# Optimization experiments

Hardware: AMD Instinct MI355X
Metric: run time of the kernel (lower is better)

Reference implementation:

```python
import jax, jax.numpy as jnp
import numpy as np
import math

B, S, DIM, H, KVH = 2, 2048, 2048, 16, 4
HD = DIM // H          # 128
G = H // KVH           # 4 (GQA repeat factor)
NEG = -1e9             # fp32 additive mask value (matches torch path)


def _rotate_half(x):
    x1, x2 = jnp.split(x, 2, axis=-1)
    return jnp.concatenate([-x2, x1], axis=-1)


def setup_inputs() -> dict:
    key = jax.random.key(0)
    ks = jax.random.split(key, 8)
    hidden_states = jax.random.normal(ks[0], (B, S, DIM), jnp.float32)
    # standard RoPE tables [S, HD]
    inv_freq = 1.0 / (10000.0 ** (jnp.arange(0, HD, 2, dtype=jnp.float32) / HD))
    freqs = jnp.outer(jnp.arange(S, dtype=jnp.float32), inv_freq)
    emb = jnp.concatenate([freqs, freqs], axis=-1)
    position_cos = jnp.cos(emb)
    position_sin = jnp.sin(emb)
    alibi_bias = jax.random.normal(ks[1], (B, S, S), jnp.float32) * 0.01
    attention_mask = jnp.zeros((B, 1, 1, S), jnp.float32)
    sc = 0.02
    wq = jax.random.normal(ks[2], (DIM, DIM), jnp.float32) * sc
    wk = jax.random.normal(ks[3], (DIM, KVH * HD), jnp.float32) * sc
    wv = jax.random.normal(ks[4], (DIM, KVH * HD), jnp.float32) * sc
    wo = jax.random.normal(ks[5], (DIM, DIM), jnp.float32) * sc
    return {"hidden_states": hidden_states, "position_cos": position_cos,
            "position_sin": position_sin, "alibi_bias": alibi_bias,
            "attention_mask": attention_mask, "wq": wq, "wk": wk, "wv": wv, "wo": wo}


def reference(hidden_states, position_cos, position_sin, alibi_bias,
              attention_mask, wq, wk, wv, wo):
    b, s, d = hidden_states.shape
    # projections (weights stored as [in, out])
    q = (hidden_states @ wq).reshape(b, s, H, HD).transpose(0, 2, 1, 3)      # [B,H,S,HD]
    k = (hidden_states @ wk).reshape(b, s, KVH, HD).transpose(0, 2, 1, 3)    # [B,KVH,S,HD]
    v = (hidden_states @ wv).reshape(b, s, KVH, HD).transpose(0, 2, 1, 3)
    # RoPE
    cos = position_cos[None, None]  # [1,1,S,HD]
    sin = position_sin[None, None]
    q = q * cos + _rotate_half(q) * sin
    k = k * cos + _rotate_half(k) * sin
    # GQA repeat kv heads
    k = jnp.repeat(k, G, axis=1)   # [B,H,S,HD]
    v = jnp.repeat(v, G, axis=1)
    scores = jnp.einsum('bhqd,bhkd->bhqk', q, k) * (1.0 / math.sqrt(HD))
    causal = jnp.triu(jnp.full((s, s), NEG, jnp.float32), 1)
    scores = scores + causal + alibi_bias[:, None, :, :] + attention_mask
    attn = jax.nn.softmax(scores.astype(jnp.float32), axis=-1).astype(q.dtype)
    out = jnp.einsum('bhqk,bhkd->bhqd', attn, v)                              # [B,H,S,HD]
    out = out.transpose(0, 2, 1, 3).reshape(b, s, d)
    return out @ wo
```

## Files before the change

### kernel.cpp

```cpp
#include <hip/hip_runtime.h>
#include <hip/hip_bf16.h>

#define Bb   2
#define Ss   2048
#define Dd   2048
#define Hh   16
#define KVHh 4
#define HDd  128

typedef __bf16 bf16x8 __attribute__((ext_vector_type(8)));
typedef float f32x4 __attribute__((ext_vector_type(4)));

__device__ __forceinline__ unsigned short f2bf(float f) {
    unsigned u = __float_as_uint(f);
    unsigned r = (u + 0x7FFFu + ((u >> 16) & 1u)) >> 16;
    return (unsigned short)r;
}
__device__ __forceinline__ float bfu2f(unsigned short u) {
    return __uint_as_float(((unsigned)u) << 16);
}

#define GLOAD16(g, l) __builtin_amdgcn_global_load_lds( \
    (const __attribute__((address_space(1))) unsigned int*)(g), \
    (__attribute__((address_space(3))) unsigned int*)(l), 16, 0, 0)

__global__ __launch_bounds__(256)
void cast_bf16(const float* __restrict__ X, unsigned short* __restrict__ Y)
{
    int idx = blockIdx.x * 256 + threadIdx.x;
    float4 v = reinterpret_cast<const float4*>(X)[idx];
    ushort4 o;
    o.x = f2bf(v.x); o.y = f2bf(v.y); o.z = f2bf(v.z); o.w = f2bf(v.w);
    reinterpret_cast<ushort4*>(Y)[idx] = o;
}

__global__ __launch_bounds__(256)
void wt_cast(const float* __restrict__ W, unsigned short* __restrict__ WT,
             int K, int N)
{
    __shared__ float tile[32][33];
    int k0 = blockIdx.x * 32, n0 = blockIdx.y * 32;
    int tx = threadIdx.x & 31, ty = threadIdx.x >> 5;
    #pragma unroll
    for (int i = 0; i < 32; i += 8)
        tile[ty + i][tx] = W[(size_t)(k0 + ty + i) * N + n0 + tx];
    __syncthreads();
    #pragma unroll
    for (int i = 0; i < 32; i += 8)
        WT[(size_t)(n0 + ty + i) * K + k0 + tx] = f2bf(tile[tx][ty + i]);
}

template<bool BF16OUT>
__global__ __launch_bounds__(256)
void gemm_bt(const unsigned short* __restrict__ A,
             const unsigned short* __restrict__ BT,
             void* __restrict__ Cv, int M, int N, int K)
{
    __shared__ __align__(16) unsigned short sA[128 * 32];
    __shared__ __align__(16) unsigned short sB[128 * 32];
    const int tid  = threadIdx.x;
    const int wave = tid >> 6;
    const int lane = tid & 63;
    const int m    = lane & 15;
    const int quad = lane >> 4;
    const int wm   = wave >> 1, wn = wave & 1;
    const int m0   = blockIdx.y * 128, n0 = blockIdx.x * 128;

    const int srow = tid >> 2;
    const int skg  = (tid & 3) * 8;

    f32x4 acc[4][4];
    #pragma unroll
    for (int r = 0; r < 4; ++r)
        #pragma unroll
        for (int c = 0; c < 4; ++c) acc[r][c] = (f32x4){0.f, 0.f, 0.f, 0.f};

    const unsigned short* pa = A  + (size_t)(m0 + srow) * K + skg;
    const unsigned short* pb = BT + (size_t)(n0 + srow) * K + skg;
    unsigned short* la = &sA[wave * 16 * 32];
    unsigned short* lb = &sB[wave * 16 * 32];

    for (int k0 = 0; k0 < K; k0 += 32) {
        GLOAD16(pa + k0, la);
        GLOAD16(pa + (size_t)64 * K + k0, la + 64 * 32);
        GLOAD16(pb + k0, lb);
        GLOAD16(pb + (size_t)64 * K + k0, lb + 64 * 32);
        __syncthreads();
        bf16x8 af[4], bfr[4];
        #pragma unroll
        for (int r = 0; r < 4; ++r)
            af[r] = *reinterpret_cast<const bf16x8*>(
                &sA[(wm * 64 + r * 16 + m) * 32 + quad * 8]);
        #pragma unroll
        for (int c = 0; c < 4; ++c)
            bfr[c] = *reinterpret_cast<const bf16x8*>(
                &sB[(wn * 64 + c * 16 + m) * 32 + quad * 8]);
        #pragma unroll
        for (int r = 0; r < 4; ++r)
            #pragma unroll
            for (int c = 0; c < 4; ++c)
                acc[r][c] = __builtin_amdgcn_mfma_f32_16x16x32_bf16(
                    af[r], bfr[c], acc[r][c], 0, 0, 0);
        __syncthreads();
    }
    #pragma unroll
    for (int r = 0; r < 4; ++r)
        #pragma unroll
        for (int c = 0; c < 4; ++c)
            #pragma unroll
            for (int e = 0; e < 4; ++e) {
                size_t row = m0 + wm * 64 + r * 16 + quad * 4 + e;
                size_t col = n0 + wn * 64 + c * 16 + m;
                if (BF16OUT)
                    ((unsigned short*)Cv)[row * N + col] = f2bf(acc[r][c][e]);
                else
                    ((float*)Cv)[row * N + col] = acc[r][c][e];
            }
}

__global__ __launch_bounds__(256)
void rope_bf(unsigned short* __restrict__ X, const float* __restrict__ cosT,
             const float* __restrict__ sinT, int nhshift, int rowstride,
             float scale, int total)
{
    int idx = blockIdx.x * 256 + threadIdx.x;
    if (idx >= total) return;
    int i   = idx & 63;
    int rh  = idx >> 6;
    int row = rh >> nhshift;
    int h   = rh & ((1 << nhshift) - 1);
    int s   = row & (Ss - 1);
    unsigned short* xp = X + (size_t)row * rowstride + h * HDd;
    float x1 = bfu2f(xp[i]);
    float x2 = bfu2f(xp[i + 64]);
    float c1 = cosT[s * HDd + i];
    float c2 = cosT[s * HDd + i + 64];
    float s1 = sinT[s * HDd + i];
    float s2 = sinT[s * HDd + i + 64];
    xp[i]      = f2bf((x1 * c1 - x2 * s1) * scale);
    xp[i + 64] = f2bf((x2 * c2 + x1 * s2) * scale);
}

__global__ __launch_bounds__(256)
void vt_cast_bf(const unsigned short* __restrict__ KV,
                unsigned short* __restrict__ VT)
{
    __shared__ unsigned short tile[32][34];
    int st = blockIdx.x * 32, dt = blockIdx.y * 32;
    int bk = blockIdx.z;
    int b = bk >> 2, kvh = bk & 3;
    int tx = threadIdx.x & 31, ty = threadIdx.x >> 5;
    #pragma unroll
    for (int i = 0; i < 32; i += 8)
        tile[ty + i][tx] = KV[(size_t)(b * Ss + st + ty + i) * 1024 + 512 + kvh * HDd + dt + tx];
    __syncthreads();
    #pragma unroll
    for (int i = 0; i < 32; i += 8)
        VT[(((size_t)b * KVHh + kvh) * HDd + dt + ty + i) * Ss + st + tx] =
            tile[tx][ty + i];
}

__global__ __launch_bounds__(256, 2)
void flash_attn(const unsigned short* __restrict__ Qb,
                const unsigned short* __restrict__ KVb,
                const unsigned short* __restrict__ VT,
                const float* __restrict__ alibi,
                const float* __restrict__ amask,
                unsigned short* __restrict__ ctx)
{
    __shared__ __align__(16) unsigned short kbuf[3][32 * 128];
    __shared__ __align__(16) unsigned short vbuf[3][128 * 32];
    __shared__ __align__(16) float          abuf[3][16 * 32];
    __shared__ __align__(16) float          am_lds[Ss];
    __shared__ unsigned short s_p[4][16][56];

    const int tid  = threadIdx.x;
    const int w    = tid >> 6;
    const int lane = tid & 63;
    const int m    = lane & 15;
    const int quad = lane >> 4;

    const int kvh = blockIdx.y;
    const int b   = blockIdx.z;
    const int h   = kvh * 4 + w;

    const unsigned short* vt0 = VT + ((size_t)b * KVHh + kvh) * HDd * Ss;
    const float* amrow = amask + (size_t)b * Ss;

    const int krow_s = tid >> 4;
    const int koff_b = ((tid & 15) * 16) ^ ((krow_s & 7) << 4);
    const int vrow_s = tid >> 2;
    const int vchk_s = (tid & 3) ^ ((vrow_s >> 1) & 3);
    const int dstw   = w * 512;

    const unsigned short* kgbase = KVb + (size_t)b * Ss * 1024 + kvh * HDd;

    {
        const float* ag = amrow + tid * 4;
        GLOAD16(ag,        am_lds + w * 256);
        GLOAD16(ag + 1024, am_lds + 1024 + w * 256);
    }

    const int qts[2] = { (int)blockIdx.x, 127 - (int)blockIdx.x };

    #pragma unroll 1
    for (int pi = 0; pi < 2; ++pi) {
        const int q0 = qts[pi] * 16;

        bf16x8 qa[4];
        {
            const unsigned short* qrow = Qb + (size_t)(b * Ss + q0 + m) * Dd + h * HDd;
            #pragma unroll
            for (int c = 0; c < 4; ++c)
                qa[c] = *reinterpret_cast<const bf16x8*>(qrow + c * 32 + quad * 8);
        }

        f32x4 o[8];
        #pragma unroll
        for (int f = 0; f < 8; ++f) o[f] = (f32x4){0.f, 0.f, 0.f, 0.f};
        float lrow[4] = {0.f, 0.f, 0.f, 0.f};

        const float* arowB = alibi + ((size_t)b * Ss + q0) * Ss;
        const int ntiles = (q0 + 47) >> 5;

        auto STAGE = [&](int kn, int buf) {
            const unsigned short* kg =
                kgbase + (size_t)(kn + krow_s) * 1024 + (koff_b >> 1);
            GLOAD16(kg,             &kbuf[buf][dstw]);
            GLOAD16(kg + 16 * 1024, &kbuf[buf][2048 + dstw]);
            const unsigned short* vg = vt0 + (size_t)vrow_s * Ss + kn + vchk_s * 8;
            GLOAD16(vg,             &vbuf[buf][dstw]);
            GLOAD16(vg + 64 * Ss,   &vbuf[buf][2048 + dstw]);
            if (tid < 128) {
                const float* ag = arowB + (size_t)(tid >> 3) * Ss + kn + (tid & 7) * 4;
                GLOAD16(ag, &abuf[buf][w * 256]);
            }
        };

        STAGE(0, 0);
        asm volatile("s_waitcnt vmcnt(0)" ::: "memory");
        __syncthreads();

        int cur = 0;
        #pragma unroll 1
        for (int kt = 0; kt < ntiles; ++kt) {
            const int k0  = kt * 32;
            const int nxt = (cur == 2) ? 0 : cur + 1;

            if (kt + 1 < ntiles) {
                STAGE(k0 + 32, nxt);
                if (w < 2) asm volatile("s_waitcnt vmcnt(5)" ::: "memory");
                else       asm volatile("s_waitcnt vmcnt(4)" ::: "memory");
            } else {
                asm volatile("s_waitcnt vmcnt(0)" ::: "memory");
            }
            __builtin_amdgcn_s_barrier();
            __builtin_amdgcn_sched_barrier(0);

            const float am0 = am_lds[k0 + m];
            const float am1 = am_lds[k0 + 16 + m];

            const char* kb  = (const char*)&kbuf[cur][0];
            const char* vbp = (const char*)&vbuf[cur][0];
            const int  ksw  = (m & 7) << 4;
            const int  vsw  = ((m >> 1) & 3) << 4;
            bf16x8 kb0[4], kb1[4];
            #pragma unroll
            for (int c = 0; c < 4; ++c) {
                kb0[c] = *(const bf16x8*)(kb + m * 256        + ((c * 64 + quad * 16) ^ ksw));
                kb1[c] = *(const bf16x8*)(kb + (16 + m) * 256 + ((c * 64 + quad * 16) ^ ksw));
            }
            f32x4 s0 = {0.f, 0.f, 0.f, 0.f}, s1 = {0.f, 0.f, 0.f, 0.f};
            #pragma unroll
            for (int c = 0; c < 4; ++c) {
                s0 = __builtin_amdgcn_mfma_f32_16x16x32_bf16(qa[c], kb0[c], s0, 0, 0, 0);
                s1 = __builtin_amdgcn_mfma_f32_16x16x32_bf16(qa[c], kb1[c], s1, 0, 0, 0);
            }

            #pragma unroll
            for (int r = 0; r < 4; ++r) {
                const int row = quad * 4 + r;
                const int qi  = q0 + row;
                float x0 = s0[r] + abuf[cur][row * 32 + m]      + am0;
                float x1 = s1[r] + abuf[cur][row * 32 + 16 + m] + am1;
                x0 = (k0 + m      <= qi) ? x0 : -1e30f;
                x1 = (k0 + 16 + m <= qi) ? x1 : -1e30f;
                const float p0 = __expf(x0);
                const float p1 = __expf(x1);
                lrow[r] += p0 + p1;
                s_p[w][row][m]      = f2bf(p0);
                s_p[w][row][16 + m] = f2bf(p1);
            }
            __builtin_amdgcn_wave_barrier();
            const bf16x8 pa = *reinterpret_cast<const bf16x8*>(&s_p[w][m][quad * 8]);
            __builtin_amdgcn_wave_barrier();

            #pragma unroll
            for (int f = 0; f < 8; ++f) {
                const bf16x8 vb = *(const bf16x8*)(vbp + (f * 16 + m) * 64 +
                                                   ((quad * 16) ^ vsw));
                o[f] = __builtin_amdgcn_mfma_f32_16x16x32_bf16(pa, vb, o[f], 0, 0, 0);
            }

            cur = nxt;
        }

        float inv[4];
        #pragma unroll
        for (int r = 0; r < 4; ++r) {
            float l = lrow[r];
            l += __shfl_xor(l, 1, 64);
            l += __shfl_xor(l, 2, 64);
            l += __shfl_xor(l, 4, 64);
            l += __shfl_xor(l, 8, 64);
            inv[r] = 1.f / l;
        }
        #pragma unroll
        for (int f = 0; f < 8; ++f)
            #pragma unroll
            for (int r = 0; r < 4; ++r)
                ctx[(size_t)(b * Ss + q0 + quad * 4 + r) * Dd + h * HDd + f * 16 + m] =
                    f2bf(o[f][r] * inv[r]);

        __syncthreads();
    }
}

extern "C" void kernel_launch(void* const* d_in, const int* in_sizes, int n_in,
                              void* d_out, int out_size, void* d_ws, size_t ws_size,
                              hipStream_t stream) {
    const float* hidden = (const float*)d_in[0];
    const float* cosT   = (const float*)d_in[1];
    const float* sinT   = (const float*)d_in[2];
    const float* alibi  = (const float*)d_in[3];
    const float* amask  = (const float*)d_in[4];
    const float* wq     = (const float*)d_in[5];
    const float* wk     = (const float*)d_in[6];
    const float* wv     = (const float*)d_in[7];
    const float* wo     = (const float*)d_in[8];
    float* out = (float*)d_out;

    char* ws = (char*)d_ws;
    unsigned short* Abf   = (unsigned short*)(ws);
    unsigned short* wqT   = (unsigned short*)(ws + 16777216);
    unsigned short* kvT   = (unsigned short*)(ws + 25165824);
    unsigned short* woT   = (unsigned short*)(ws + 29360128);
    unsigned short* Qraw  = (unsigned short*)(ws + 37748736);
    unsigned short* KVraw = (unsigned short*)(ws + 54525952);
    unsigned short* VT    = (unsigned short*)(ws + 62914560);
    unsigned short* Ctx   = (unsigned short*)(ws + 67108864);

    const int M = Bb * Ss;

    cast_bf16<<<(M * Dd / 4) / 256, 256, 0, stream>>>(hidden, Abf);
    wt_cast<<<dim3(64, 64), 256, 0, stream>>>(wq, wqT, Dd, Dd);
    wt_cast<<<dim3(64, 16), 256, 0, stream>>>(wk, kvT, Dd, 512);
    wt_cast<<<dim3(64, 16), 256, 0, stream>>>(wv, kvT + (size_t)512 * Dd, Dd, 512);
    wt_cast<<<dim3(64, 64), 256, 0, stream>>>(wo, woT, Dd, Dd);

    gemm_bt<true><<<dim3(Dd / 128, M / 128), 256, 0, stream>>>(Abf, wqT, Qraw, M, Dd, Dd);
    gemm_bt<true><<<dim3(1024 / 128, M / 128), 256, 0, stream>>>(Abf, kvT, KVraw, M, 1024, Dd);

    const float scale = 0.08838834764831845f;
    int totQ = Bb * Ss * Hh * 64;
    rope_bf<<<totQ / 256, 256, 0, stream>>>(Qraw, cosT, sinT, 4, Dd, scale, totQ);
    int totK = Bb * Ss * KVHh * 64;
    rope_bf<<<totK / 256, 256, 0, stream>>>(KVraw, cosT, sinT, 2, 1024, 1.0f, totK);

    vt_cast_bf<<<dim3(Ss / 32, HDd / 32, Bb * KVHh), 256, 0, stream>>>(KVraw, VT);

    flash_attn<<<dim3(64, KVHh, Bb), 256, 0, stream>>>(Qraw, KVraw, VT, alibi, amask, Ctx);

    gemm_bt<false><<<dim3(Dd / 128, M / 128), 256, 0, stream>>>(Ctx, woT, out, M, Dd, Dd);
}
```

Baseline: 417.4 us.

## Fuse QKV projection, merge weight casts and RoPE, interleave paired query tiles

Merges the four weight-transpose launches into one kernel and the Q and KV projections into a single GEMM with a combined 3072-wide output. The two RoPE launches become one kernel over that shared buffer. The attention kernel now processes its two query tiles (short and long) together in one K/V loop, reusing each staged K/V tile and its fragments for both, and reorders block-to-tile mapping by batch. This cuts kernel launches and halves K/V LDS traffic for the short tile, at the cost of higher register pressure from two accumulator sets.

```diff
diff --git a/kernel.cpp b/kernel.cpp
--- a/kernel.cpp
+++ b/kernel.cpp
@@ -7,6 +7,7 @@
 #define Hh   16
 #define KVHh 4
 #define HDd  128
+#define QKVW 3072
 
 typedef __bf16 bf16x8 __attribute__((ext_vector_type(8)));
 typedef float f32x4 __attribute__((ext_vector_type(4)));
@@ -35,11 +36,19 @@
 }
 
 __global__ __launch_bounds__(256)
-void wt_cast(const float* __restrict__ W, unsigned short* __restrict__ WT,
-             int K, int N)
+void wt_cast_all(const float* __restrict__ wq, const float* __restrict__ wk,
+                 const float* __restrict__ wv, const float* __restrict__ wo,
+                 unsigned short* __restrict__ wqkvT, unsigned short* __restrict__ woT)
 {
     __shared__ float tile[32][33];
-    int k0 = blockIdx.x * 32, n0 = blockIdx.y * 32;
+    int id = blockIdx.x;
+    const float* W; unsigned short* WT; int N, kx, ny;
+    if (id < 4096)      {            W = wq; WT = wqkvT;                        N = 2048; kx = id & 63; ny = id >> 6; }
+    else if (id < 5120) { id -= 4096; W = wk; WT = wqkvT + (size_t)2048 * 2048; N = 512;  kx = id & 63; ny = id >> 6; }
+    else if (id < 6144) { id -= 5120; W = wv; WT = wqkvT + (size_t)2560 * 2048; N = 512;  kx = id & 63; ny = id >> 6; }
+    else                { id -= 6144; W = wo; WT = woT;                         N = 2048; kx = id & 63; ny = id >> 6; }
+    const int K = 2048;
+    int k0 = kx * 32, n0 = ny * 32;
     int tx = threadIdx.x & 31, ty = threadIdx.x >> 5;
     #pragma unroll
     for (int i = 0; i < 32; i += 8)
@@ -119,18 +128,15 @@
 }
 
 __global__ __launch_bounds__(256)
-void rope_bf(unsigned short* __restrict__ X, const float* __restrict__ cosT,
-             const float* __restrict__ sinT, int nhshift, int rowstride,
-             float scale, int total)
-{
-    int idx = blockIdx.x * 256 + threadIdx.x;
-    if (idx >= total) return;
-    int i   = idx & 63;
-    int rh  = idx >> 6;
-    int row = rh >> nhshift;
-    int h   = rh & ((1 << nhshift) - 1);
-    int s   = row & (Ss - 1);
-    unsigned short* xp = X + (size_t)row * rowstride + h * HDd;
+void rope_all(unsigned short* __restrict__ qkv, const float* __restrict__ cosT,
+              const float* __restrict__ sinT)
+{
+    const int h   = blockIdx.y;
+    const int row = blockIdx.x * 4 + (threadIdx.x >> 6);
+    const int i   = threadIdx.x & 63;
+    const int s   = row & (Ss - 1);
+    const float scale = (h < Hh) ? 0.08838834764831845f : 1.0f;
+    unsigned short* xp = qkv + (size_t)row * QKVW + h * HDd;
     float x1 = bfu2f(xp[i]);
     float x2 = bfu2f(xp[i + 64]);
     float c1 = cosT[s * HDd + i];
@@ -152,7 +158,7 @@
     int tx = threadIdx.x & 31, ty = threadIdx.x >> 5;
     #pragma unroll
     for (int i = 0; i < 32; i += 8)
-        tile[ty + i][tx] = KV[(size_t)(b * Ss + st + ty + i) * 1024 + 512 + kvh * HDd + dt + tx];
+        tile[ty + i][tx] = KV[(size_t)(b * Ss + st + ty + i) * QKVW + 2560 + kvh * HDd + dt + tx];
     __syncthreads();
     #pragma unroll
     for (int i = 0; i < 32; i += 8)
@@ -161,8 +167,7 @@
 }
 
 __global__ __launch_bounds__(256, 2)
-void flash_attn(const unsigned short* __restrict__ Qb,
-                const unsigned short* __restrict__ KVb,
+void flash_attn(const unsigned short* __restrict__ qkv,
                 const unsigned short* __restrict__ VT,
                 const float* __restrict__ alibi,
                 const float* __restrict__ amask,
@@ -170,22 +175,32 @@
 {
     __shared__ __align__(16) unsigned short kbuf[3][32 * 128];
     __shared__ __align__(16) unsigned short vbuf[3][128 * 32];
-    __shared__ __align__(16) float          abuf[3][16 * 32];
+    __shared__ __align__(16) float          abuf[3][2][512];
     __shared__ __align__(16) float          am_lds[Ss];
     __shared__ unsigned short s_p[4][16][56];
 
     const int tid  = threadIdx.x;
     const int w    = tid >> 6;
-    const int lane = tid & 63;
-    const int m    = lane & 15;
-    const int quad = lane >> 4;
+    const int m    = tid & 15;
+    const int quad = (tid & 63) >> 4;
 
     const int kvh = blockIdx.y;
     const int b   = blockIdx.z;
     const int h   = kvh * 4 + w;
 
+    const int x    = blockIdx.x;
+    const int qtA0 = (x & 1) ? (63 - (x >> 1)) : (x >> 1);
+    const int qtA  = b ? (63 - qtA0) : qtA0;
+    const int qtB  = 127 - qtA;
+    const int qA0  = qtA * 16, qB0 = qtB * 16;
+    const int ntA  = (qA0 + 47) >> 5;
+    const int ntB  = (qB0 + 47) >> 5;
+
     const unsigned short* vt0 = VT + ((size_t)b * KVHh + kvh) * HDd * Ss;
     const float* amrow = amask + (size_t)b * Ss;
+    const float* arowA = alibi + ((size_t)b * Ss + qA0) * Ss;
+    const float* arowB = alibi + ((size_t)b * Ss + qB0) * Ss;
+    const unsigned short* kgbase = qkv + (size_t)b * Ss * QKVW + 2048 + kvh * HDd;
 
     const int krow_s = tid >> 4;
     const int koff_b = ((tid & 15) * 16) ^ ((krow_s & 7) << 4);
@@ -193,137 +208,171 @@
     const int vchk_s = (tid & 3) ^ ((vrow_s >> 1) & 3);
     const int dstw   = w * 512;
 
-    const unsigned short* kgbase = KVb + (size_t)b * Ss * 1024 + kvh * HDd;
-
     {
         const float* ag = amrow + tid * 4;
         GLOAD16(ag,        am_lds + w * 256);
         GLOAD16(ag + 1024, am_lds + 1024 + w * 256);
     }
-
-    const int qts[2] = { (int)blockIdx.x, 127 - (int)blockIdx.x };
-
+    bf16x8 qaA[4], qaB[4];
+    {
+        const unsigned short* qrA = qkv + (size_t)(b * Ss + qA0 + m) * QKVW + h * HDd;
+        const unsigned short* qrB = qkv + (size_t)(b * Ss + qB0 + m) * QKVW + h * HDd;
+        #pragma unroll
+        for (int c = 0; c < 4; ++c) {
+            qaA[c] = *reinterpret_cast<const bf16x8*>(qrA + c * 32 + quad * 8);
+            qaB[c] = *reinterpret_cast<const bf16x8*>(qrB + c * 32 + quad * 8);
+        }
+    }
+
+    f32x4 oA[8], oB[8];
+    #pragma unroll
+    for (int f = 0; f < 8; ++f) {
+        oA[f] = (f32x4){0.f, 0.f, 0.f, 0.f};
+        oB[f] = (f32x4){0.f, 0.f, 0.f, 0.f};
+    }
+    float lA[4] = {0.f, 0.f, 0.f, 0.f}, lB[4] = {0.f, 0.f, 0.f, 0.f};
+
+    auto STAGE = [&](int kn, int buf, bool aact) {
+        const unsigned short* kg =
+            kgbase + (size_t)(kn + krow_s) * QKVW + (koff_b >> 1);
+        GLOAD16(kg,              &kbuf[buf][dstw]);
+        GLOAD16(kg + 16 * QKVW,  &kbuf[buf][2048 + dstw]);
+        const unsigned short* vg = vt0 + (size_t)vrow_s * Ss + kn + vchk_s * 8;
+        GLOAD16(vg,             &vbuf[buf][dstw]);
+        GLOAD16(vg + 64 * Ss,   &vbuf[buf][2048 + dstw]);
+        if (tid < 128) {
+            if (aact) {
+                const float* ag = arowA + (size_t)(tid >> 3) * Ss + kn + (tid & 7) * 4;
+                GLOAD16(ag, &abuf[buf][0][w * 256]);
+            }
+        } else {
+            const float* ag = arowB + (size_t)((tid - 128) >> 3) * Ss + kn + (tid & 7) * 4;
+            GLOAD16(ag, &abuf[buf][1][(w - 2) * 256]);
+        }
+    };
+
+    STAGE(0, 0, true);
+    asm volatile("s_waitcnt vmcnt(0)" ::: "memory");
+    __syncthreads();
+
+    int cur = 0;
     #pragma unroll 1
-    for (int pi = 0; pi < 2; ++pi) {
-        const int q0 = qts[pi] * 16;
-
-        bf16x8 qa[4];
+    for (int kt = 0; kt < ntB; ++kt) {
+        const int k0  = kt * 32;
+        const int nxt = (cur == 2) ? 0 : cur + 1;
+        const bool aact = kt < ntA;
+
+        if (kt + 1 < ntB) {
+            const bool aactn = (kt + 1) < ntA;
+            STAGE(k0 + 32, nxt, aactn);
+            if (w < 2) {
+                if (aactn) asm volatile("s_waitcnt vmcnt(5)" ::: "memory");
+                else       asm volatile("s_waitcnt vmcnt(4)" ::: "memory");
+            } else       asm volatile("s_waitcnt vmcnt(5)" ::: "memory");
+        } else {
+            asm volatile("s_waitcnt vmcnt(0)" ::: "memory");
+        }
+        __builtin_amdgcn_s_barrier();
+        __builtin_amdgcn_sched_barrier(0);
+
+        const float am0 = am_lds[k0 + m];
+        const float am1 = am_lds[k0 + 16 + m];
+
+        const char* kb  = (const char*)&kbuf[cur][0];
+        const char* vbp = (const char*)&vbuf[cur][0];
+        const int  ksw  = (m & 7) << 4;
+        const int  vsw  = ((m >> 1) & 3) << 4;
+        bf16x8 kf0[4], kf1[4];
+        #pragma unroll
+        for (int c = 0; c < 4; ++c) {
+            kf0[c] = *(const bf16x8*)(kb + m * 256        + ((c * 64 + quad * 16) ^ ksw));
+            kf1[c] = *(const bf16x8*)(kb + (16 + m) * 256 + ((c * 64 + quad * 16) ^ ksw));
+        }
+        bf16x8 vf[8];
+        #pragma unroll
+        for (int f = 0; f < 8; ++f)
+            vf[f] = *(const bf16x8*)(vbp + (f * 16 + m) * 64 + ((quad * 16) ^ vsw));
+
         {
-            const unsigned short* qrow = Qb + (size_t)(b * Ss + q0 + m) * Dd + h * HDd;
-            #pragma unroll
-            for (int c = 0; c < 4; ++c)
-                qa[c] = *reinterpret_cast<const bf16x8*>(qrow + c * 32 + quad * 8);
-        }
-
-        f32x4 o[8];
-        #pragma unroll
-        for (int f = 0; f < 8; ++f) o[f] = (f32x4){0.f, 0.f, 0.f, 0.f};
-        float lrow[4] = {0.f, 0.f, 0.f, 0.f};
-
-        const float* arowB = alibi + ((size_t)b * Ss + q0) * Ss;
-        const int ntiles = (q0 + 47) >> 5;
-
-        auto STAGE = [&](int kn, int buf) {
-            const unsigned short* kg =
-                kgbase + (size_t)(kn + krow_s) * 1024 + (koff_b >> 1);
-            GLOAD16(kg,             &kbuf[buf][dstw]);
-            GLOAD16(kg + 16 * 1024, &kbuf[buf][2048 + dstw]);
-            const unsigned short* vg = vt0 + (size_t)vrow_s * Ss + kn + vchk_s * 8;
-            GLOAD16(vg,             &vbuf[buf][dstw]);
-            GLOAD16(vg + 64 * Ss,   &vbuf[buf][2048 + dstw]);
-            if (tid < 128) {
-                const float* ag = arowB + (size_t)(tid >> 3) * Ss + kn + (tid & 7) * 4;
-                GLOAD16(ag, &abuf[buf][w * 256]);
-            }
-        };
-
-        STAGE(0, 0);
-        asm volatile("s_waitcnt vmcnt(0)" ::: "memory");
-        __syncthreads();
-
-        int cur = 0;
-        #pragma unroll 1
-        for (int kt = 0; kt < ntiles; ++kt) {
-            const int k0  = kt * 32;
-            const int nxt = (cur == 2) ? 0 : cur + 1;
-
-            if (kt + 1 < ntiles) {
-                STAGE(k0 + 32, nxt);
-                if (w < 2) asm volatile("s_waitcnt vmcnt(5)" ::: "memory");
-                else       asm volatile("s_waitcnt vmcnt(4)" ::: "memory");
-            } else {
-                asm volatile("s_waitcnt vmcnt(0)" ::: "memory");
-            }
-            __builtin_amdgcn_s_barrier();
-            __builtin_amdgcn_sched_barrier(0);
-
-            const float am0 = am_lds[k0 + m];
-            const float am1 = am_lds[k0 + 16 + m];
-
-            const char* kb  = (const char*)&kbuf[cur][0];
-            const char* vbp = (const char*)&vbuf[cur][0];
-            const int  ksw  = (m & 7) << 4;
-            const int  vsw  = ((m >> 1) & 3) << 4;
-            bf16x8 kb0[4], kb1[4];
+            f32x4 s0 = {0.f, 0.f, 0.f, 0.f}, s1 = {0.f, 0.f, 0.f, 0.f};
             #pragma unroll
             for (int c = 0; c < 4; ++c) {
-                kb0[c] = *(const bf16x8*)(kb + m * 256        + ((c * 64 + quad * 16) ^ ksw));
-                kb1[c] = *(const bf16x8*)(kb + (16 + m) * 256 + ((c * 64 + quad * 16) ^ ksw));
-            }
-            f32x4 s0 = {0.f, 0.f, 0.f, 0.f}, s1 = {0.f, 0.f, 0.f, 0.f};
-            #pragma unroll
-            for (int c = 0; c < 4; ++c) {
-                s0 = __builtin_amdgcn_mfma_f32_16x16x32_bf16(qa[c], kb0[c], s0, 0, 0, 0);
-                s1 = __builtin_amdgcn_mfma_f32_16x16x32_bf16(qa[c], kb1[c], s1, 0, 0, 0);
-            }
-
+                s0 = __builtin_amdgcn_mfma_f32_16x16x32_bf16(qaB[c], kf0[c], s0, 0, 0, 0);
+                s1 = __builtin_amdgcn_mfma_f32_16x16x32_bf16(qaB[c], kf1[c], s1, 0, 0, 0);
+            }
             #pragma unroll
             for (int r = 0; r < 4; ++r) {
                 const int row = quad * 4 + r;
-                const int qi  = q0 + row;
-                float x0 = s0[r] + abuf[cur][row * 32 + m]      + am0;
-                float x1 = s1[r] + abuf[cur][row * 32 + 16 + m] + am1;
+                const int qi  = qB0 + row;
+                float x0 = s0[r] + abuf[cur][1][row * 32 + m]      + am0;
+                float x1 = s1[r] + abuf[cur][1][row * 32 + 16 + m] + am1;
                 x0 = (k0 + m      <= qi) ? x0 : -1e30f;
                 x1 = (k0 + 16 + m <= qi) ? x1 : -1e30f;
                 const float p0 = __expf(x0);
                 const float p1 = __expf(x1);
-                lrow[r] += p0 + p1;
+                lB[r] += p0 + p1;
                 s_p[w][row][m]      = f2bf(p0);
                 s_p[w][row][16 + m] = f2bf(p1);
             }
             __builtin_amdgcn_wave_barrier();
             const bf16x8 pa = *reinterpret_cast<const bf16x8*>(&s_p[w][m][quad * 8]);
             __builtin_amdgcn_wave_barrier();
-
-            #pragma unroll
-            for (int f = 0; f < 8; ++f) {
-                const bf16x8 vb = *(const bf16x8*)(vbp + (f * 16 + m) * 64 +
-                                                   ((quad * 16) ^ vsw));
-                o[f] = __builtin_amdgcn_mfma_f32_16x16x32_bf16(pa, vb, o[f], 0, 0, 0);
-            }
-
-            cur = nxt;
-        }
-
-        float inv[4];
+            #pragma unroll
+            for (int f = 0; f < 8; ++f)
+                oB[f] = __builtin_amdgcn_mfma_f32_16x16x32_bf16(pa, vf[f], oB[f], 0, 0, 0);
+        }
+
+        if (aact) {
+            f32x4 s0 = {0.f, 0.f, 0.f, 0.f}, s1 = {0.f, 0.f, 0.f, 0.f};
+            #pragma unroll
+            for (int c = 0; c < 4; ++c) {
+                s0 = __builtin_amdgcn_mfma_f32_16x16x32_bf16(qaA[c], kf0[c], s0, 0, 0, 0);
+                s1 = __builtin_amdgcn_mfma_f32_16x16x32_bf16(qaA[c], kf1[c], s1, 0, 0, 0);
+            }
+            #pragma unroll
+            for (int r = 0; r < 4; ++r) {
+                const int row = quad * 4 + r;
+                const int qi  = qA0 + row;
+                float x0 = s0[r] + abuf[cur][0][row * 32 + m]      + am0;
+                float x1 = s1[r] + abuf[cur][0][row * 32 + 16 + m] + am1;
+                x0 = (k0 + m      <= qi) ? x0 : -1e30f;
+                x1 = (k0 + 16 + m <= qi) ? x1 : -1e30f;
+                const float p0 = __expf(x0);
+                const float p1 = __expf(x1);
+                lA[r] += p0 + p1;
+                s_p[w][row][m]      = f2bf(p0);
+                s_p[w][row][16 + m] = f2bf(p1);
+            }
+            __builtin_amdgcn_wave_barrier();
+            const bf16x8 pa = *reinterpret_cast<const bf16x8*>(&s_p[w][m][quad * 8]);
+            __builtin_amdgcn_wave_barrier();
+            #pragma unroll
+            for (int f = 0; f < 8; ++f)
+                oA[f] = __builtin_amdgcn_mfma_f32_16x16x32_bf16(pa, vf[f], oA[f], 0, 0, 0);
+        }
+
+        cur = nxt;
+    }
+
+    float invA[4], invB[4];
+    #pragma unroll
+    for (int r = 0; r < 4; ++r) {
+        float la = lA[r], lb = lB[r];
+        la += __shfl_xor(la, 1, 64); lb += __shfl_xor(lb, 1, 64);
+        la += __shfl_xor(la, 2, 64); lb += __shfl_xor(lb, 2, 64);
+        la += __shfl_xor(la, 4, 64); lb += __shfl_xor(lb, 4, 64);
+        la += __shfl_xor(la, 8, 64); lb += __shfl_xor(lb, 8, 64);
+        invA[r] = 1.f / la; invB[r] = 1.f / lb;
+    }
+    #pragma unroll
+    for (int f = 0; f < 8; ++f)
         #pragma unroll
         for (int r = 0; r < 4; ++r) {
-            float l = lrow[r];
-            l += __shfl_xor(l, 1, 64);
-            l += __shfl_xor(l, 2, 64);
-            l += __shfl_xor(l, 4, 64);
-            l += __shfl_xor(l, 8, 64);
-            inv[r] = 1.f / l;
-        }
-        #pragma unroll
-        for (int f = 0; f < 8; ++f)
-            #pragma unroll
-            for (int r = 0; r < 4; ++r)
-                ctx[(size_t)(b * Ss + q0 + quad * 4 + r) * Dd + h * HDd + f * 16 + m] =
-                    f2bf(o[f][r] * inv[r]);
-
-        __syncthreads();
-    }
+            ctx[(size_t)(b * Ss + qA0 + quad * 4 + r) * Dd + h * HDd + f * 16 + m] =
+                f2bf(oA[f][r] * invA[r]);
+            ctx[(size_t)(b * Ss + qB0 + quad * 4 + r) * Dd + h * HDd + f * 16 + m] =
+                f2bf(oB[f][r] * invB[r]);
+        }
 }
 
 extern "C" void kernel_launch(void* const* d_in, const int* in_sizes, int n_in,
@@ -341,35 +390,25 @@
     float* out = (float*)d_out;
 
     char* ws = (char*)d_ws;
-    unsigned short* Abf   = (unsigned short*)(ws);
-    unsigned short* wqT   = (unsigned short*)(ws + 16777216);
-    unsigned short* kvT   = (unsigned short*)(ws + 25165824);
-    unsigned short* woT   = (unsigned short*)(ws + 29360128);
-    unsigned short* Qraw  = (unsigned short*)(ws + 37748736);
-    unsigned short* KVraw = (unsigned short*)(ws + 54525952);
-    unsigned short* VT    = (unsigned short*)(ws + 62914560);
-    unsigned short* Ctx   = (unsigned short*)(ws + 67108864);
+    unsigned short* Abf    = (unsigned short*)(ws);
+    unsigned short* wqkvT  = (unsigned short*)(ws + 16777216);
+    unsigned short* woT    = (unsigned short*)(ws + 29360128);
+    unsigned short* QKVraw = (unsigned short*)(ws + 37748736);
+    unsigned short* VT     = (unsigned short*)(ws + 62914560);
+    unsigned short* Ctx    = (unsigned short*)(ws + 67108864);
 
     const int M = Bb * Ss;
 
     cast_bf16<<<(M * Dd / 4) / 256, 256, 0, stream>>>(hidden, Abf);
-    wt_cast<<<dim3(64, 64), 256, 0, stream>>>(wq, wqT, Dd, Dd);
-    wt_cast<<<dim3(64, 16), 256, 0, stream>>>(wk, kvT, Dd, 512);
-    wt_cast<<<dim3(64, 16), 256, 0, stream>>>(wv, kvT + (size_t)512 * Dd, Dd, 512);
-    wt_cast<<<dim3(64, 64), 256, 0, stream>>>(wo, woT, Dd, Dd);
-
-    gemm_bt<true><<<dim3(Dd / 128, M / 128), 256, 0, stream>>>(Abf, wqT, Qraw, M, Dd, Dd);
-    gemm_bt<true><<<dim3(1024 / 128, M / 128), 256, 0, stream>>>(Abf, kvT, KVraw, M, 1024, Dd);
-
-    const float scale = 0.08838834764831845f;
-    int totQ = Bb * Ss * Hh * 64;
-    rope_bf<<<totQ / 256, 256, 0, stream>>>(Qraw, cosT, sinT, 4, Dd, scale, totQ);
-    int totK = Bb * Ss * KVHh * 64;
-    rope_bf<<<totK / 256, 256, 0, stream>>>(KVraw, cosT, sinT, 2, 1024, 1.0f, totK);
-
-    vt_cast_bf<<<dim3(Ss / 32, HDd / 32, Bb * KVHh), 256, 0, stream>>>(KVraw, VT);
-
-    flash_attn<<<dim3(64, KVHh, Bb), 256, 0, stream>>>(Qraw, KVraw, VT, alibi, amask, Ctx);
+    wt_cast_all<<<10240, 256, 0, stream>>>(wq, wk, wv, wo, wqkvT, woT);
+
+    gemm_bt<true><<<dim3(QKVW / 128, M / 128), 256, 0, stream>>>(Abf, wqkvT, QKVraw, M, QKVW, Dd);
+
+    rope_all<<<dim3(M / 4, 20), 256, 0, stream>>>(QKVraw, cosT, sinT);
+
+    vt_cast_bf<<<dim3(Ss / 32, HDd / 32, Bb * KVHh), 256, 0, stream>>>(QKVraw, VT);
+
+    flash_attn<<<dim3(64, KVHh, Bb), 256, 0, stream>>>(QKVraw, VT, alibi, amask, Ctx);
 
     gemm_bt<false><<<dim3(Dd / 128, M / 128), 256, 0, stream>>>(Ctx, woT, out, M, Dd, Dd);
 }
```

Measured after the change: 363.2 us. 13.0% less time.
